# Kernel optimization log

Hardware: AMD Instinct MI355X
Metric: run time of the kernel (lower is better)

The kernel has to match this reference:

```python
import jax, jax.numpy as jnp
from jax import lax
import numpy as np

B, T, H = 128, 512, 512  # batch, seq_length, hidden_dim (== input_dim)


def _xavier(key, shape):
    fan_in, fan_out = shape[1], shape[0]
    limit = float(np.sqrt(6.0 / (fan_in + fan_out)))
    return jax.random.uniform(key, shape, jnp.float32, -limit, limit)


def setup_inputs() -> dict:
    key = jax.random.key(0)
    ks = jax.random.split(key, 10)
    s = 1.0 / np.sqrt(H)  # torch LSTM default init range
    return {
        "x": jax.random.normal(ks[0], (B, T, H), jnp.float32),
        "W_ih": jax.random.uniform(ks[1], (4 * H, H), jnp.float32, -s, s),
        "W_hh": jax.random.uniform(ks[2], (4 * H, H), jnp.float32, -s, s),
        "b_ih": jax.random.uniform(ks[3], (4 * H,), jnp.float32, -s, s),
        "b_hh": jax.random.uniform(ks[4], (4 * H,), jnp.float32, -s, s),
        "Ve": _xavier(ks[5], (1, H)),
        "U1": _xavier(ks[6], (H, 2 * H)),
        "U2": _xavier(ks[7], (H, H)),
        "W_out": _xavier(ks[8], (2, H)),
        "b_out": jnp.zeros((2,), jnp.float32),
    }


def _lstm(x, W_ih, W_hh, b_ih, b_hh):
    # x: [B, T, D] -> hidden states [B, T, H]; PyTorch gate order i,f,g,o
    b = b_ih + b_hh
    # precompute input projections for all timesteps: [T, B, 4H]
    xg = jnp.einsum('btd,gd->tbg', x, W_ih) + b

    def step(carry, xt):
        h, c = carry
        g = xt + h @ W_hh.T  # [B, 4H]
        i, f, gg, o = jnp.split(g, 4, axis=1)
        c = jax.nn.sigmoid(f) * c + jax.nn.sigmoid(i) * jnp.tanh(gg)
        h = jax.nn.sigmoid(o) * jnp.tanh(c)
        return (h, c), h

    h0 = jnp.zeros((x.shape[0], W_hh.shape[1]), x.dtype)
    (_, _), hs = lax.scan(step, (h0, h0), xg)
    return jnp.swapaxes(hs, 0, 1)  # [B, T, H]


def reference(x, W_ih, W_hh, b_ih, b_hh, Ve, U1, U2, W_out, b_out):
    h = _lstm(x, W_ih, W_hh, b_ih, b_hh)  # [B, T, H]
    h_last = h[:, -1, :]  # [B, H]
    # additive attention, vectorized over all timesteps
    Hdim = h.shape[-1]
    u1 = jnp.einsum('bth,gh->btg', h, U1[:, :Hdim]) + jnp.einsum('bh,gh->bg', h_last, U1[:, Hdim:])[:, None, :]
    u2 = jnp.einsum('btd,gd->btg', x, U2)
    u = jnp.tanh(u1 + u2)  # [B, T, H]
    e = jnp.einsum('bth,h->bt', u, Ve[0])
    alpha = jax.nn.softmax(e, axis=1)  # [B, T]
    context = jnp.einsum('bt,bth->bh', alpha, h)  # [B, H]
    params = context @ W_out.T + b_out  # [B, 2]
    mu = params[:, 0]
    sigma = jax.nn.softplus(params[:, 1]) + 1e-5
    return (mu, sigma)
```

## Files before the change

kernel.cpp:

```cpp
#include <hip/hip_runtime.h>
#include <stdint.h>


using short8  = __attribute__((ext_vector_type(8))) short;
using short4v = __attribute__((ext_vector_type(4))) short;
using floatx4 = __attribute__((ext_vector_type(4))) float;

#define MFMA16(a, b, c) __builtin_amdgcn_mfma_f32_16x16x32_bf16((a), (b), (c), 0, 0, 0)

__device__ __forceinline__ unsigned short f2b(float f) {
    unsigned u = __float_as_uint(f);
    u += 0x7FFFu + ((u >> 16) & 1u);
    return (unsigned short)(u >> 16);
}
__device__ __forceinline__ float b2f(unsigned short h) {
    return __uint_as_float(((unsigned)h) << 16);
}
__device__ __forceinline__ float sigm(float x) { return 1.0f / (1.0f + __expf(-x)); }
__device__ __forceinline__ float tanh_(float x) { return 1.0f - 2.0f / (__expf(2.0f * x) + 1.0f); }

__global__ __launch_bounds__(256) void prep(
    const float* __restrict__ x, const float* __restrict__ Wih, const float* __restrict__ Whh,
    const float* __restrict__ bih, const float* __restrict__ bhh,
    const float* __restrict__ U1, const float* __restrict__ U2,
    unsigned short* __restrict__ x_bf, unsigned short* __restrict__ Wih_bf,
    unsigned short* __restrict__ Whh_bf, unsigned short* __restrict__ U1a,
    unsigned short* __restrict__ U1b, unsigned short* __restrict__ U2b,
    float* __restrict__ bias)
{
    const long long NX4 = 33554432LL / 4;
    const long long NREST = 1048576LL + 1048576LL + 524288LL + 262144LL + 2048LL;
    const long long total = NX4 + NREST;
    for (long long u = (long long)blockIdx.x * 256 + threadIdx.x; u < total;
         u += (long long)gridDim.x * 256) {
        if (u < NX4) {
            float4 v = ((const float4*)x)[u];
            short4v o;
            o[0] = (short)f2b(v.x); o[1] = (short)f2b(v.y);
            o[2] = (short)f2b(v.z); o[3] = (short)f2b(v.w);
            *(short4v*)&x_bf[u * 4] = o;
        } else {
            long long i = u - NX4;
            if (i < 1048576) { Wih_bf[i] = f2b(Wih[i]); continue; }
            i -= 1048576;
            if (i < 1048576) { Whh_bf[i] = f2b(Whh[i]); continue; }
            i -= 1048576;
            if (i < 524288) {
                int row = (int)(i >> 10), col = (int)(i & 1023);
                if (col < 512) U1a[row * 512 + col] = f2b(U1[i]);
                else           U1b[row * 512 + (col - 512)] = f2b(U1[i]);
                continue;
            }
            i -= 524288;
            if (i < 262144) { U2b[i] = f2b(U2[i]); continue; }
            i -= 262144;
            bias[i] = bih[i] + bhh[i];
        }
    }
}

__device__ __forceinline__ void gemm_core(
    const unsigned short* __restrict__ A, long long lda,
    const unsigned short* __restrict__ Bm, long long ldb,
    unsigned short* __restrict__ C, long long ldc,
    const float* __restrict__ bias, int mode,
    int m0, int n0, int tid, unsigned short* sbuf)
{
    unsigned short* At = sbuf;
    unsigned short* Bt = sbuf + 128 * 72;
    unsigned short* Ct = sbuf;

    const int wv = tid >> 6, lane = tid & 63, l15 = lane & 15, q = lane >> 4;
    const int wm = wv & 1, wn = wv >> 1;

    floatx4 acc[4][4];
    for (int i = 0; i < 4; i++)
        for (int j = 0; j < 4; j++) acc[i][j] = (floatx4){0.f, 0.f, 0.f, 0.f};

    for (int k0 = 0; k0 < 512; k0 += 64) {
        for (int p = 0; p < 4; p++) {
            int idx = tid + p * 256;
            int row = idx >> 3, ch = idx & 7;
            *(short8*)&At[row * 72 + ch * 8] =
                *(const short8*)&A[(long long)(m0 + row) * lda + k0 + ch * 8];
            *(short8*)&Bt[row * 72 + ch * 8] =
                *(const short8*)&Bm[(long long)(n0 + row) * ldb + k0 + ch * 8];
        }
        __syncthreads();
        for (int ks = 0; ks < 64; ks += 32) {
            short8 af[4], bfv[4];
            for (int mi = 0; mi < 4; mi++)
                af[mi] = *(const short8*)&At[(wm * 64 + mi * 16 + l15) * 72 + ks + q * 8];
            for (int ni = 0; ni < 4; ni++)
                bfv[ni] = *(const short8*)&Bt[(wn * 64 + ni * 16 + l15) * 72 + ks + q * 8];
            for (int mi = 0; mi < 4; mi++)
                for (int ni = 0; ni < 4; ni++)
                    acc[mi][ni] = MFMA16(af[mi], bfv[ni], acc[mi][ni]);
        }
        __syncthreads();
    }

    float bv[4];
    for (int ni = 0; ni < 4; ni++)
        bv[ni] = bias ? bias[n0 + wn * 64 + ni * 16 + l15] : 0.0f;

    for (int mi = 0; mi < 4; mi++)
        for (int ni = 0; ni < 4; ni++)
            for (int r = 0; r < 4; r++)
                Ct[(wm * 64 + mi * 16 + q * 4 + r) * 128 + wn * 64 + ni * 16 + l15] =
                    f2b(acc[mi][ni][r] + bv[ni]);
    __syncthreads();

    const int tt0 = m0 & 511, bglob = m0 >> 9;
    for (int p = 0; p < 8; p++) {
        int idx = tid + p * 256;
        int row = idx >> 4, ch = idx & 15;
        if (mode) {
            int n = n0 + ch * 8;
            int gate = n >> 9, jg = (n >> 4) & 31, c0 = gate * 16 + (n & 15);
            long long dst = (((long long)(tt0 + row) * 32 + jg) * 128 + bglob) * 64 + c0;
            *(short8*)&C[dst] = *(const short8*)&Ct[row * 128 + ch * 8];
        } else {
            *(short8*)&C[(long long)(m0 + row) * ldc + n0 + ch * 8] =
                *(const short8*)&Ct[row * 128 + ch * 8];
        }
    }
}

__global__ __launch_bounds__(256) void gemm_bt(
    const unsigned short* __restrict__ A, long long lda,
    const unsigned short* __restrict__ Bm, long long ldb,
    unsigned short* __restrict__ C, long long ldc,
    const float* __restrict__ bias, int mode, int mmul)
{
    __shared__ __align__(16) unsigned short sbuf[2 * 128 * 72];
    gemm_core(A, lda, Bm, ldb, C, ldc, bias, mode,
              blockIdx.x * mmul, blockIdx.y * 128, threadIdx.x, sbuf);
}

template<int NNI>
__device__ __forceinline__ void attn_helper_body(
    const unsigned short* __restrict__ h_all,
    const unsigned short* __restrict__ x_bf,
    const unsigned short* __restrict__ U1a,
    const unsigned short* __restrict__ U2b,
    unsigned short* __restrict__ xg_out,
    int* __restrict__ syncp,
    int b, int t0, int nBase, int tid, char* smem)
{
    const int bg = b >> 4;
    if (tid < 8) {
        while (__hip_atomic_load(&syncp[16 + (bg * 8 + tid) * 16],
                                 __ATOMIC_RELAXED,
                                 __HIP_MEMORY_SCOPE_AGENT) < t0 + 32)
            __builtin_amdgcn_s_sleep(8);
    }
    __syncthreads();

    unsigned short* Bt2 = (unsigned short*)smem;
    unsigned short* At2 = (unsigned short*)smem + (NNI * 64) * 40;

    const int wv = tid >> 6, lane = tid & 63, l15 = lane & 15, q = lane >> 4;

    floatx4 acc[2][NNI];
    #pragma unroll
    for (int mi = 0; mi < 2; mi++)
        #pragma unroll
        for (int ni = 0; ni < NNI; ni++) acc[mi][ni] = (floatx4){0.f, 0.f, 0.f, 0.f};

    for (int it = 0; it < 32; it++) {
        const int phase = it >> 4, kk = (it & 15) * 32;
        const unsigned short* Bsrc = phase ? U2b : U1a;
        __syncthreads();
        #pragma unroll
        for (int pp = 0; pp < NNI; pp++) {
            int idx = tid + pp * 256;
            int row = idx >> 2, ch = idx & 3;
            *(short8*)&Bt2[row * 40 + ch * 8] =
                *(const short8*)&Bsrc[(long long)(nBase + row) * 512 + kk + ch * 8];
        }
        if (tid < 128) {
            int row = tid >> 2, ch = tid & 3;
            if (phase == 0) {
                unsigned long long* p = (unsigned long long*)
                    &h_all[((long long)b * 512 + t0 + row) * 512 + kk + ch * 8];
                unsigned long long lo = __hip_atomic_load(p, __ATOMIC_RELAXED,
                                                          __HIP_MEMORY_SCOPE_AGENT);
                unsigned long long hi = __hip_atomic_load(p + 1, __ATOMIC_RELAXED,
                                                          __HIP_MEMORY_SCOPE_AGENT);
                unsigned long long* d = (unsigned long long*)&At2[row * 40 + ch * 8];
                d[0] = lo; d[1] = hi;
            } else {
                *(short8*)&At2[row * 40 + ch * 8] =
                    *(const short8*)&x_bf[((long long)b * 512 + t0 + row) * 512 + kk + ch * 8];
            }
        }
        __syncthreads();
        short8 af0 = *(const short8*)&At2[(l15) * 40 + q * 8];
        short8 af1 = *(const short8*)&At2[(16 + l15) * 40 + q * 8];
        #pragma unroll
        for (int ni = 0; ni < NNI; ni++) {
            short8 bfv = *(const short8*)&Bt2[(wv * (NNI * 16) + ni * 16 + l15) * 40 + q * 8];
            acc[0][ni] = MFMA16(af0, bfv, acc[0][ni]);
            acc[1][ni] = MFMA16(af1, bfv, acc[1][ni]);
        }
    }
    #pragma unroll
    for (int mi = 0; mi < 2; mi++)
        #pragma unroll
        for (int ni = 0; ni < NNI; ni++) {
            const int n = nBase + wv * (NNI * 16) + ni * 16 + l15;
            #pragma unroll
            for (int r = 0; r < 4; r++) {
                const int t = t0 + mi * 16 + q * 4 + r;
                float* slot = (float*)&xg_out[(((long long)t * 32 + (n >> 5)) * 128 + b) * 64];
                slot[n & 31] = acc[mi][ni][r];
            }
        }
}

#define GEMM_WGS 6144
#define ATTN_WGS 2432
__global__ __launch_bounds__(256, 1) void mega(
    const unsigned short* __restrict__ xg,
    const unsigned short* __restrict__ Whh,
    unsigned short* __restrict__ h_all,
    unsigned int* __restrict__ ring,
    const unsigned short* __restrict__ x_bf,
    const unsigned short* __restrict__ Wih_bf,
    const float* __restrict__ bias,
    unsigned short* __restrict__ xg_out,
    int* __restrict__ syncp,
    const unsigned short* __restrict__ U1a,
    const unsigned short* __restrict__ U2b)
{
    __shared__ __align__(16) char smem[86016];

    const int tid = threadIdx.x;

    if (blockIdx.x >= 64 && blockIdx.x < 64 + GEMM_WGS) {
        int g = blockIdx.x - 64;
        int b = g & 127;
        int r = g >> 7;
        int ti = 1 + (r % 3);
        int n = r / 3;
        gemm_core(x_bf, 512, Wih_bf, 512, xg_out, 2048, bias, 1,
                  b * 512 + ti * 128, n * 128, tid, (unsigned short*)smem);
        __syncthreads();
        if (tid == 0)
            __hip_atomic_fetch_add(&syncp[0], 1, __ATOMIC_RELEASE,
                                   __HIP_MEMORY_SCOPE_AGENT);
        return;
    }

    if (blockIdx.x >= 64 + GEMM_WGS) {
        const int g = blockIdx.x - 64 - GEMM_WGS;
        if (g < 1920) {
            attn_helper_body<8>(h_all, x_bf, U1a, U2b, xg_out, syncp,
                                g & 127, (g >> 7) * 32, 0, tid, smem);
        } else {
            const int j = g - 1920;
            attn_helper_body<2>(h_all, x_bf, U1a, U2b, xg_out, syncp,
                                j & 127, 480, (j >> 7) * 128, tid, smem);
        }
        return;
    }

    unsigned int (*At)[16 * 264] = (unsigned int (*)[16 * 264])smem;

    const int wv = tid >> 6, lane = tid & 63, l15 = lane & 15, q = lane >> 4;
    const int bg = blockIdx.x >> 3, jgb = blockIdx.x & 7;
    const int b0 = bg * 16;
    const int jg32 = jgb * 4 + wv;
    const int hid = jg32 * 16 + l15;

    short8 Wreg[4][16];
    #pragma unroll
    for (int ct = 0; ct < 4; ct++)
        #pragma unroll
        for (int kk = 0; kk < 16; kk++)
            Wreg[ct][kk] = *(const short8*)
                &Whh[(long long)(ct * 512 + hid) * 512 + kk * 32 + q * 8];

    float cst[4] = {0.f, 0.f, 0.f, 0.f};

    for (int t = 0; t < 512; t++) {
        if (t == 128) {
            if (tid == 0) {
                while (__hip_atomic_load(&syncp[0], __ATOMIC_ACQUIRE,
                                         __HIP_MEMORY_SCOPE_AGENT) < GEMM_WGS)
                    __builtin_amdgcn_s_sleep(8);
            }
            __syncthreads();
        }
        const long long xbase = ((long long)(t * 32 + jg32) * 128 + b0) * 64;
        floatx4 acc[4];
        #pragma unroll
        for (int ct = 0; ct < 4; ct++)
            #pragma unroll
            for (int r = 0; r < 4; r++)
                acc[ct][r] = b2f(xg[xbase + (q * 4 + r) * 64 + ct * 16 + l15]);

        if (t > 0) {
            const unsigned want = (unsigned)(t - 1);
            const int sl = (t - 1) & 1;
            unsigned long long* rb = (unsigned long long*)
                (ring + sl * 65536 + b0 * 512);
            unsigned long long w[16];
            #pragma unroll
            for (int i = 0; i < 16; i++)
                w[i] = __hip_atomic_load(&rb[tid + i * 256], __ATOMIC_RELAXED,
                                         __HIP_MEMORY_SCOPE_AGENT);
            while (true) {
                unsigned bad = 0;
                #pragma unroll
                for (int i = 0; i < 16; i++) {
                    unsigned lo = (unsigned)(w[i] >> 16) & 0xFFFFu;
                    unsigned hi = (unsigned)(w[i] >> 48);
                    bad |= (lo ^ want) | (hi ^ want);
                }
                if (!bad) break;
                #pragma unroll
                for (int i = 0; i < 16; i++) {
                    unsigned lo = (unsigned)(w[i] >> 16) & 0xFFFFu;
                    unsigned hi = (unsigned)(w[i] >> 48);
                    if ((lo ^ want) | (hi ^ want))
                        w[i] = __hip_atomic_load(&rb[tid + i * 256], __ATOMIC_RELAXED,
                                                 __HIP_MEMORY_SCOPE_AGENT);
                }
            }
            unsigned int* dst = &At[sl][0];
            #pragma unroll
            for (int i = 0; i < 16; i++) {
                int idx = tid + i * 256;
                int row = idx >> 8, k = idx & 255;
                dst[row * 264 + k] =
                    (unsigned)(w[i] & 0xFFFFu) | ((unsigned)(w[i] >> 32) << 16);
            }
            __syncthreads();
            const unsigned int* ap = &At[sl][l15 * 264 + q * 4];
            #pragma unroll
            for (int kk = 0; kk < 16; kk++) {
                short8 af = *(const short8*)(ap + kk * 16);
                acc[0] = MFMA16(af, Wreg[0][kk], acc[0]);
                acc[1] = MFMA16(af, Wreg[1][kk], acc[1]);
                acc[2] = MFMA16(af, Wreg[2][kk], acc[2]);
                acc[3] = MFMA16(af, Wreg[3][kk], acc[3]);
            }
        }
        unsigned short hbv[4];
        #pragma unroll
        for (int r = 0; r < 4; r++) {
            float ig = sigm(acc[0][r]);
            float fg = sigm(acc[1][r]);
            float gv = tanh_(acc[2][r]);
            float og = sigm(acc[3][r]);
            cst[r] = fg * cst[r] + ig * gv;
            hbv[r] = f2b(og * tanh_(cst[r]));
        }
        #pragma unroll
        for (int r = 0; r < 4; r++) {
            const int b = b0 + q * 4 + r;
            __hip_atomic_store(&ring[(t & 1) * 65536 + b * 512 + hid],
                               ((unsigned)t << 16) | hbv[r], __ATOMIC_RELAXED,
                               __HIP_MEMORY_SCOPE_AGENT);
        }
        #pragma unroll
        for (int r = 0; r < 4; r++) {
            const int b = b0 + q * 4 + r;
            int o = __shfl_xor((int)hbv[r], 1);
            if (!(l15 & 1)) {
                unsigned v = (unsigned)hbv[r] | (((unsigned)(unsigned short)o) << 16);
                __hip_atomic_store(
                    (unsigned*)&h_all[(long long)b * 262144 + (long long)t * 512 + hid],
                    v, __ATOMIC_RELAXED, __HIP_MEMORY_SCOPE_AGENT);
            }
        }
        if ((t & 15) == 15) {
            __syncthreads();
            if (tid == 0)
                __hip_atomic_store(&syncp[16 + (int)blockIdx.x * 16], t + 1,
                                   __ATOMIC_RELAXED, __HIP_MEMORY_SCOPE_AGENT);
        }
    }
}

__global__ __launch_bounds__(256) void attn_out(
    const unsigned short* __restrict__ a_xg,
    const unsigned short* __restrict__ h_all,
    const unsigned short* __restrict__ U1b,
    const float* __restrict__ Ve,
    const float* __restrict__ Wout, const float* __restrict__ bout,
    float* __restrict__ outp)
{
    __shared__ float hl[512];
    __shared__ float u1s[512];
    __shared__ float se[512];
    __shared__ float sm[512];
    __shared__ float red[8];
    const int b = blockIdx.x, tid = threadIdx.x;
    const int wv = tid >> 6, lane = tid & 63;

    {
        unsigned v = ((const unsigned*)(h_all + (long long)b * 262144 + 511LL * 512))[tid];
        hl[2 * tid]     = b2f((unsigned short)(v & 0xFFFFu));
        hl[2 * tid + 1] = b2f((unsigned short)(v >> 16));
    }
    __syncthreads();
    #pragma unroll
    for (int rr = 0; rr < 2; rr++) {
        const int n = tid + rr * 256;
        const unsigned short* up = &U1b[(long long)n * 512];
        float s = 0.f;
        for (int k = 0; k < 512; k += 8) {
            short8 v8 = *(const short8*)&up[k];
            #pragma unroll
            for (int j = 0; j < 8; j++)
                s += hl[k + j] * b2f((unsigned short)v8[j]);
        }
        u1s[n] = s;
    }
    __syncthreads();

    const int n0 = lane * 8;
    float ve[8], ub[8];
    #pragma unroll
    for (int j = 0; j < 8; j++) {
        ve[j] = Ve[n0 + j];
        ub[j] = u1s[n0 + j];
    }
    for (int it = 0; it < 64; it++) {
        const int t = it * 8 + wv * 2;
        const float* s0p = (const float*)
            &a_xg[(((long long)t * 32 + (n0 >> 5)) * 128 + b) * 64];
        const float* s1p = (const float*)
            &a_xg[(((long long)(t + 1) * 32 + (n0 >> 5)) * 128 + b) * 64];
        float4 a0 = *(const float4*)&s0p[n0 & 31];
        float4 a1 = *(const float4*)&s0p[(n0 & 31) + 4];
        float4 a2 = *(const float4*)&s1p[n0 & 31];
        float4 a3 = *(const float4*)&s1p[(n0 & 31) + 4];
        float s0 = ve[0] * tanh_(a0.x + ub[0]) + ve[1] * tanh_(a0.y + ub[1])
                 + ve[2] * tanh_(a0.z + ub[2]) + ve[3] * tanh_(a0.w + ub[3])
                 + ve[4] * tanh_(a1.x + ub[4]) + ve[5] * tanh_(a1.y + ub[5])
                 + ve[6] * tanh_(a1.z + ub[6]) + ve[7] * tanh_(a1.w + ub[7]);
        float s1 = ve[0] * tanh_(a2.x + ub[0]) + ve[1] * tanh_(a2.y + ub[1])
                 + ve[2] * tanh_(a2.z + ub[2]) + ve[3] * tanh_(a2.w + ub[3])
                 + ve[4] * tanh_(a3.x + ub[4]) + ve[5] * tanh_(a3.y + ub[5])
                 + ve[6] * tanh_(a3.z + ub[6]) + ve[7] * tanh_(a3.w + ub[7]);
        #pragma unroll
        for (int off = 1; off <= 32; off <<= 1) {
            s0 += __shfl_xor(s0, off);
            s1 += __shfl_xor(s1, off);
        }
        if (lane == 0) { se[t] = s0; se[t + 1] = s1; }
    }
    __syncthreads();

    float e0 = se[tid], e1 = se[256 + tid];
    float mx = fmaxf(e0, e1);
    for (int off = 32; off; off >>= 1) mx = fmaxf(mx, __shfl_xor(mx, off));
    if (lane == 0) red[wv] = mx;
    __syncthreads();
    mx = fmaxf(fmaxf(red[0], red[1]), fmaxf(red[2], red[3]));

    float s0 = __expf(e0 - mx), s1 = __expf(e1 - mx);
    sm[tid] = s0; sm[256 + tid] = s1;
    float ss = s0 + s1;
    for (int off = 32; off; off >>= 1) ss += __shfl_xor(ss, off);
    if (lane == 0) red[4 + wv] = ss;
    __syncthreads();
    float inv = 1.0f / (red[4] + red[5] + red[6] + red[7]);

    const unsigned int* hp = (const unsigned int*)(h_all + (long long)b * 262144);
    float a0 = 0.f, a1 = 0.f;
    for (int t = 0; t < 512; t += 4) {
        #pragma unroll
        for (int j = 0; j < 4; j++) {
            float al = sm[t + j];
            unsigned v = hp[(t + j) * 256 + tid];
            a0 += al * b2f((unsigned short)(v & 0xFFFFu));
            a1 += al * b2f((unsigned short)(v >> 16));
        }
    }
    a0 *= inv; a1 *= inv;

    float q0 = a0 * Wout[2 * tid] + a1 * Wout[2 * tid + 1];
    float q1 = a0 * Wout[512 + 2 * tid] + a1 * Wout[512 + 2 * tid + 1];
    for (int off = 32; off; off >>= 1) { q0 += __shfl_xor(q0, off); q1 += __shfl_xor(q1, off); }
    __syncthreads();
    if (lane == 0) { red[wv] = q0; red[4 + wv] = q1; }
    __syncthreads();
    if (tid == 0) {
        float P0 = red[0] + red[1] + red[2] + red[3] + bout[0];
        float P1 = red[4] + red[5] + red[6] + red[7] + bout[1];
        outp[b] = P0;
        float sp = (P1 > 15.0f) ? P1 : log1pf(__expf(P1));
        outp[128 + b] = sp + 1e-5f;
    }
}

extern "C" void kernel_launch(void* const* d_in, const int* in_sizes, int n_in,
                              void* d_out, int out_size, void* d_ws, size_t ws_size,
                              hipStream_t stream)
{
    const float* x    = (const float*)d_in[0];
    const float* Wih  = (const float*)d_in[1];
    const float* Whh  = (const float*)d_in[2];
    const float* bih  = (const float*)d_in[3];
    const float* bhh  = (const float*)d_in[4];
    const float* Ve   = (const float*)d_in[5];
    const float* U1   = (const float*)d_in[6];
    const float* U2   = (const float*)d_in[7];
    const float* Wout = (const float*)d_in[8];
    const float* bout = (const float*)d_in[9];
    float* out = (float*)d_out;

    char* ws = (char*)d_ws;
    size_t off = 0;
    auto alloc = [&](size_t bytes) -> void* {
        void* p = ws + off;
        off += (bytes + 255) & ~(size_t)255;
        return p;
    };
    unsigned short* x_bf   = (unsigned short*)alloc(33554432ull * 2);
    unsigned short* Wih_bf = (unsigned short*)alloc(1048576ull * 2);
    unsigned short* Whh_bf = (unsigned short*)alloc(1048576ull * 2);
    unsigned short* U1a    = (unsigned short*)alloc(262144ull * 2);
    unsigned short* U1b    = (unsigned short*)alloc(262144ull * 2);
    unsigned short* U2b    = (unsigned short*)alloc(262144ull * 2);
    float*          bias   = (float*)alloc(2048ull * 4);
    unsigned short* xg     = (unsigned short*)alloc(134217728ull * 2);
    unsigned short* h_all  = (unsigned short*)alloc(33554432ull * 2);
    unsigned int*   ring   = (unsigned int*)alloc(131072ull * 4);
    int*            syncp  = (int*)alloc(8192ull);
    if (off > ws_size) return;

    hipMemsetAsync(syncp, 0, 8192, stream);
    prep<<<4096, 256, 0, stream>>>(x, Wih, Whh, bih, bhh, U1, U2,
                                   x_bf, Wih_bf, Whh_bf, U1a, U1b, U2b, bias);
    gemm_bt<<<dim3(128, 16), 256, 0, stream>>>(x_bf, 512, Wih_bf, 512,
                                               xg, 2048, bias, 1, 512);
    mega<<<64 + GEMM_WGS + ATTN_WGS, 256, 0, stream>>>(
        xg, Whh_bf, h_all, ring, x_bf, Wih_bf, bias, xg, syncp, U1a, U2b);
    attn_out<<<128, 256, 0, stream>>>(xg, h_all, U1b, Ve, Wout, bout, out);
}
```

Before: 2.567 ms.

## Fuse x bf16 conversion into input-projection GEMM and overlap remaining conversions

Splits the prep kernel. A small kernel now converts only W_ih and sums the biases. A fused kernel then runs the input-projection GEMM reading fp32 x directly, converting it to bf16 while staging into LDS. The same launch uses extra workgroups to convert x, W_hh and U1/U2 to bf16 in parallel with the GEMM. This removes the dependency of the GEMM on a full x conversion pass and overlaps conversion with compute, at the cost of reading fp32 x twice and having the GEMM and conversion workgroups compete for bandwidth.

```diff
diff --git a/kernel.cpp b/kernel.cpp
--- a/kernel.cpp
+++ b/kernel.cpp
@@ -19,43 +19,16 @@
 __device__ __forceinline__ float sigm(float x) { return 1.0f / (1.0f + __expf(-x)); }
 __device__ __forceinline__ float tanh_(float x) { return 1.0f - 2.0f / (__expf(2.0f * x) + 1.0f); }
 
-__global__ __launch_bounds__(256) void prep(
-    const float* __restrict__ x, const float* __restrict__ Wih, const float* __restrict__ Whh,
-    const float* __restrict__ bih, const float* __restrict__ bhh,
-    const float* __restrict__ U1, const float* __restrict__ U2,
-    unsigned short* __restrict__ x_bf, unsigned short* __restrict__ Wih_bf,
-    unsigned short* __restrict__ Whh_bf, unsigned short* __restrict__ U1a,
-    unsigned short* __restrict__ U1b, unsigned short* __restrict__ U2b,
-    float* __restrict__ bias)
-{
-    const long long NX4 = 33554432LL / 4;
-    const long long NREST = 1048576LL + 1048576LL + 524288LL + 262144LL + 2048LL;
-    const long long total = NX4 + NREST;
-    for (long long u = (long long)blockIdx.x * 256 + threadIdx.x; u < total;
-         u += (long long)gridDim.x * 256) {
-        if (u < NX4) {
-            float4 v = ((const float4*)x)[u];
-            short4v o;
-            o[0] = (short)f2b(v.x); o[1] = (short)f2b(v.y);
-            o[2] = (short)f2b(v.z); o[3] = (short)f2b(v.w);
-            *(short4v*)&x_bf[u * 4] = o;
-        } else {
-            long long i = u - NX4;
-            if (i < 1048576) { Wih_bf[i] = f2b(Wih[i]); continue; }
-            i -= 1048576;
-            if (i < 1048576) { Whh_bf[i] = f2b(Whh[i]); continue; }
-            i -= 1048576;
-            if (i < 524288) {
-                int row = (int)(i >> 10), col = (int)(i & 1023);
-                if (col < 512) U1a[row * 512 + col] = f2b(U1[i]);
-                else           U1b[row * 512 + (col - 512)] = f2b(U1[i]);
-                continue;
-            }
-            i -= 524288;
-            if (i < 262144) { U2b[i] = f2b(U2[i]); continue; }
-            i -= 262144;
-            bias[i] = bih[i] + bhh[i];
-        }
+__global__ __launch_bounds__(256) void prep_w(
+    const float* __restrict__ Wih, const float* __restrict__ bih,
+    const float* __restrict__ bhh,
+    unsigned short* __restrict__ Wih_bf, float* __restrict__ bias)
+{
+    const int total = 1048576 + 2048;
+    for (int i = blockIdx.x * 256 + threadIdx.x; i < total;
+         i += gridDim.x * 256) {
+        if (i < 1048576) Wih_bf[i] = f2b(Wih[i]);
+        else             bias[i - 1048576] = bih[i - 1048576] + bhh[i - 1048576];
     }
 }
 
@@ -127,15 +100,121 @@
     }
 }
 
-__global__ __launch_bounds__(256) void gemm_bt(
-    const unsigned short* __restrict__ A, long long lda,
-    const unsigned short* __restrict__ Bm, long long ldb,
-    unsigned short* __restrict__ C, long long ldc,
-    const float* __restrict__ bias, int mode, int mmul)
+__device__ __forceinline__ void gemm_core_xf32(
+    const float* __restrict__ Af, long long lda,
+    const unsigned short* __restrict__ Bm,
+    unsigned short* __restrict__ C,
+    const float* __restrict__ bias,
+    int m0, int n0, int tid, unsigned short* sbuf)
+{
+    unsigned short* At = sbuf;
+    unsigned short* Bt = sbuf + 128 * 72;
+    unsigned short* Ct = sbuf;
+
+    const int wv = tid >> 6, lane = tid & 63, l15 = lane & 15, q = lane >> 4;
+    const int wm = wv & 1, wn = wv >> 1;
+
+    floatx4 acc[4][4];
+    for (int i = 0; i < 4; i++)
+        for (int j = 0; j < 4; j++) acc[i][j] = (floatx4){0.f, 0.f, 0.f, 0.f};
+
+    for (int k0 = 0; k0 < 512; k0 += 64) {
+        for (int p = 0; p < 4; p++) {
+            int idx = tid + p * 256;
+            int row = idx >> 3, ch = idx & 7;
+            const float* ap = &Af[(long long)(m0 + row) * lda + k0 + ch * 8];
+            float4 v0 = *(const float4*)ap;
+            float4 v1 = *(const float4*)(ap + 4);
+            short8 o;
+            o[0] = (short)f2b(v0.x); o[1] = (short)f2b(v0.y);
+            o[2] = (short)f2b(v0.z); o[3] = (short)f2b(v0.w);
+            o[4] = (short)f2b(v1.x); o[5] = (short)f2b(v1.y);
+            o[6] = (short)f2b(v1.z); o[7] = (short)f2b(v1.w);
+            *(short8*)&At[row * 72 + ch * 8] = o;
+            *(short8*)&Bt[row * 72 + ch * 8] =
+                *(const short8*)&Bm[(long long)(n0 + row) * 512 + k0 + ch * 8];
+        }
+        __syncthreads();
+        for (int ks = 0; ks < 64; ks += 32) {
+            short8 af[4], bfv[4];
+            for (int mi = 0; mi < 4; mi++)
+                af[mi] = *(const short8*)&At[(wm * 64 + mi * 16 + l15) * 72 + ks + q * 8];
+            for (int ni = 0; ni < 4; ni++)
+                bfv[ni] = *(const short8*)&Bt[(wn * 64 + ni * 16 + l15) * 72 + ks + q * 8];
+            for (int mi = 0; mi < 4; mi++)
+                for (int ni = 0; ni < 4; ni++)
+                    acc[mi][ni] = MFMA16(af[mi], bfv[ni], acc[mi][ni]);
+        }
+        __syncthreads();
+    }
+
+    float bv[4];
+    for (int ni = 0; ni < 4; ni++)
+        bv[ni] = bias[n0 + wn * 64 + ni * 16 + l15];
+
+    for (int mi = 0; mi < 4; mi++)
+        for (int ni = 0; ni < 4; ni++)
+            for (int r = 0; r < 4; r++)
+                Ct[(wm * 64 + mi * 16 + q * 4 + r) * 128 + wn * 64 + ni * 16 + l15] =
+                    f2b(acc[mi][ni][r] + bv[ni]);
+    __syncthreads();
+
+    const int tt0 = m0 & 511, bglob = m0 >> 9;
+    for (int p = 0; p < 8; p++) {
+        int idx = tid + p * 256;
+        int row = idx >> 4, ch = idx & 15;
+        int n = n0 + ch * 8;
+        int gate = n >> 9, jg = (n >> 4) & 31, c0 = gate * 16 + (n & 15);
+        long long dst = (((long long)(tt0 + row) * 32 + jg) * 128 + bglob) * 64 + c0;
+        *(short8*)&C[dst] = *(const short8*)&Ct[row * 128 + ch * 8];
+    }
+}
+
+#define CONV_WGS 512
+__global__ __launch_bounds__(256) void gemm_fused(
+    const float* __restrict__ x, const float* __restrict__ Whh,
+    const float* __restrict__ U1, const float* __restrict__ U2,
+    unsigned short* __restrict__ x_bf, unsigned short* __restrict__ Whh_bf,
+    unsigned short* __restrict__ U1a, unsigned short* __restrict__ U1b,
+    unsigned short* __restrict__ U2b,
+    const unsigned short* __restrict__ Wih_bf, const float* __restrict__ bias,
+    unsigned short* __restrict__ xg_out)
 {
     __shared__ __align__(16) unsigned short sbuf[2 * 128 * 72];
-    gemm_core(A, lda, Bm, ldb, C, ldc, bias, mode,
-              blockIdx.x * mmul, blockIdx.y * 128, threadIdx.x, sbuf);
+    const int tid = threadIdx.x;
+
+    if (blockIdx.x < CONV_WGS) {
+        const long long NX4 = 33554432LL / 4;
+        const long long NREST = 1048576LL + 524288LL + 262144LL;
+        const long long total = NX4 + NREST;
+        for (long long u = (long long)blockIdx.x * 256 + tid; u < total;
+             u += (long long)CONV_WGS * 256) {
+            if (u < NX4) {
+                float4 v = ((const float4*)x)[u];
+                short4v o;
+                o[0] = (short)f2b(v.x); o[1] = (short)f2b(v.y);
+                o[2] = (short)f2b(v.z); o[3] = (short)f2b(v.w);
+                *(short4v*)&x_bf[u * 4] = o;
+            } else {
+                long long i = u - NX4;
+                if (i < 1048576) { Whh_bf[i] = f2b(Whh[i]); continue; }
+                i -= 1048576;
+                if (i < 524288) {
+                    int row = (int)(i >> 10), col = (int)(i & 1023);
+                    if (col < 512) U1a[row * 512 + col] = f2b(U1[i]);
+                    else           U1b[row * 512 + (col - 512)] = f2b(U1[i]);
+                    continue;
+                }
+                i -= 524288;
+                U2b[i] = f2b(U2[i]);
+            }
+        }
+        return;
+    }
+
+    const int g = blockIdx.x - CONV_WGS;
+    const int b = g & 127, n = g >> 7;
+    gemm_core_xf32(x, 512, Wih_bf, xg_out, bias, b * 512, n * 128, tid, sbuf);
 }
 
 template<int NNI>
@@ -536,10 +615,9 @@
     if (off > ws_size) return;
 
     hipMemsetAsync(syncp, 0, 8192, stream);
-    prep<<<4096, 256, 0, stream>>>(x, Wih, Whh, bih, bhh, U1, U2,
-                                   x_bf, Wih_bf, Whh_bf, U1a, U1b, U2b, bias);
-    gemm_bt<<<dim3(128, 16), 256, 0, stream>>>(x_bf, 512, Wih_bf, 512,
-                                               xg, 2048, bias, 1, 512);
+    prep_w<<<1024, 256, 0, stream>>>(Wih, bih, bhh, Wih_bf, bias);
+    gemm_fused<<<CONV_WGS + 2048, 256, 0, stream>>>(
+        x, Whh, U1, U2, x_bf, Whh_bf, U1a, U1b, U2b, Wih_bf, bias, xg);
     mega<<<64 + GEMM_WGS + ATTN_WGS, 256, 0, stream>>>(
         xg, Whh_bf, h_all, ring, x_bf, Wih_bf, bias, xg, syncp, U1a, U2b);
     attn_out<<<128, 256, 0, stream>>>(xg, h_all, U1b, Ve, Wout, bout, out);
```

New measurement: 2.592 ms. About the same (+1.0%).
